# Kernel tuning notes

Measured on AMD Instinct MI355X. Metric: run time of the kernel, lower is better.

The kernel has to match this reference:

```python
import jax, jax.numpy as jnp
import numpy as np

B, LX, LY, D = 8, 2048, 2048, 256

def setup_inputs() -> dict:
    key = jax.random.key(0)
    k1, k2, k3, k4 = jax.random.split(key, 4)
    x = jax.random.normal(k1, (B, LX, D), dtype=jnp.float32)
    y = jax.random.normal(k2, (B, LY, D), dtype=jnp.float32)
    y_mask = jax.random.randint(k3, (B, LY), 0, 2).astype(jnp.bool_)
    W = jax.random.normal(k4, (D, D), dtype=jnp.float32) * (1.0 / np.sqrt(D))
    b = jnp.zeros((D,), dtype=jnp.float32)
    return {"x": x, "y": y, "y_mask": y_mask, "W": W, "b": b}

def reference(x, y, y_mask, W, b):
    # shared linear + relu projection (torch Linear: x @ W.T + b)
    x_proj = jax.nn.relu(jnp.einsum('bld,ed->ble', x, W) + b)  # [B,LX,D]
    y_proj = jax.nn.relu(jnp.einsum('bld,ed->ble', y, W) + b)  # [B,LY,D]
    scores = jnp.einsum('bxd,byd->bxy', x_proj, y_proj)        # [B,LX,LY]
    scores = jnp.where(y_mask[:, None, :], -jnp.inf, scores)
    alpha = jax.nn.softmax(scores, axis=-1)                    # [B,LX,LY]
    return jnp.einsum('bxy,byd->bxd', alpha, y)                # [B,LX,D]
```

## Files before the change

kernel.cpp:

```cpp
#include <hip/hip_runtime.h>

typedef __attribute__((ext_vector_type(8))) short short8;
typedef _Float16 half8 __attribute__((ext_vector_type(8)));
typedef __attribute__((ext_vector_type(4))) float f32x4;
typedef __attribute__((ext_vector_type(4))) unsigned int uint4v;
typedef __attribute__((ext_vector_type(2))) unsigned int uint2v;

#define B_   8
#define LX_  2048
#define LY_  2048
#define D_   256
#define NROW (B_ * LX_)

__device__ __forceinline__ unsigned short f2bf(float f) {
  unsigned u = __builtin_bit_cast(unsigned, f);
  u += 0x7FFF + ((u >> 16) & 1);
  return (unsigned short)(u >> 16);
}
__device__ __forceinline__ float bf2f(unsigned short h) {
  unsigned u = ((unsigned)h) << 16;
  return __builtin_bit_cast(float, u);
}

__global__ __launch_bounds__(256) void prep_kernel(
    const float* __restrict__ W, unsigned short* __restrict__ Whi,
    unsigned short* __restrict__ Wlo,
    const int* __restrict__ MASK, int* __restrict__ CIDX, int* __restrict__ Lc) {
  int t = threadIdx.x;
  if (blockIdx.x >= 8) {
    int base = (blockIdx.x - 8) * 2048 + t * 8;
    f32x4 f0 = *(const f32x4*)(W + base);
    f32x4 f1 = *(const f32x4*)(W + base + 4);
    float v[8] = {f0[0], f0[1], f0[2], f0[3], f1[0], f1[1], f1[2], f1[3]};
    unsigned short h[8], l[8];
    for (int j = 0; j < 8; ++j) {
      h[j] = f2bf(v[j]);
      l[j] = f2bf(v[j] - bf2f(h[j]));
    }
    uint4v vh = {(unsigned)h[0] | ((unsigned)h[1] << 16), (unsigned)h[2] | ((unsigned)h[3] << 16),
                 (unsigned)h[4] | ((unsigned)h[5] << 16), (unsigned)h[6] | ((unsigned)h[7] << 16)};
    uint4v vl = {(unsigned)l[0] | ((unsigned)l[1] << 16), (unsigned)l[2] | ((unsigned)l[3] << 16),
                 (unsigned)l[4] | ((unsigned)l[5] << 16), (unsigned)l[6] | ((unsigned)l[7] << 16)};
    *(uint4v*)(Whi + base) = vh;
    *(uint4v*)(Wlo + base) = vl;
    return;
  }
  __shared__ int s[256];
  int b = blockIdx.x;
  int f[8];
  int cnt = 0;
  for (int k = 0; k < 8; ++k) {
    f[k] = (MASK[b * 2048 + t * 8 + k] == 0) ? 1 : 0;
    cnt += f[k];
  }
  s[t] = cnt;
  __syncthreads();
  for (int off = 1; off < 256; off <<= 1) {
    int v = (t >= off) ? s[t - off] : 0;
    __syncthreads();
    s[t] += v;
    __syncthreads();
  }
  if (t == 255) Lc[b] = s[255];
  int off = s[t] - cnt;
  for (int k = 0; k < 8; ++k) {
    int j = t * 8 + k;
    if (f[k]) CIDX[b * 2048 + (off++)] = j;
  }
}

__global__ __launch_bounds__(256, 2) void projgather_kernel(
    const float* __restrict__ X, const float* __restrict__ Y,
    const float* __restrict__ bias,
    const unsigned short* __restrict__ Whi, const unsigned short* __restrict__ Wlo,
    const int* __restrict__ CIDX, const int* __restrict__ Lc,
    _Float16* __restrict__ XP, _Float16* __restrict__ YPc,
    _Float16* __restrict__ YTc) {
  __shared__ __align__(16) unsigned char smem[51200];
  int t = threadIdx.x;

  if (blockIdx.x >= 512) {
    _Float16 (*tile)[72] = (_Float16(*)[72])smem;
    int id = blockIdx.x - 512;
    int db = id & 3, nb = (id >> 2) & 31, b = id >> 7;
    int lc = Lc[b];
    int end = (lc + 31) & ~31;
    if (nb * 64 >= end) return;
    int nl = t >> 2, ds = t & 3;
    int j = nb * 64 + nl;
    int idx = (j < lc) ? CIDX[b * 2048 + j] : 0;
    const float* src = Y + (size_t)(b * LY_ + idx) * D_ + db * 64 + ds * 16;
    for (int i = 0; i < 4; ++i) {
      f32x4 f = *(const f32x4*)(src + i * 4);
      for (int k = 0; k < 4; ++k) tile[ds * 16 + i * 4 + k][nl] = (_Float16)f[k];
    }
    __syncthreads();
    int dl = t >> 2, nsub = t & 3;
    uint4v v0 = *(const uint4v*)&tile[dl][nsub * 16];
    uint4v v1 = *(const uint4v*)&tile[dl][nsub * 16 + 8];
    _Float16* dst = YTc + (size_t)(b * D_ + db * 64 + dl) * LY_ + nb * 64 + nsub * 16;
    *(uint4v*)(dst) = v0;
    *(uint4v*)(dst + 8) = v1;
    return;
  }

  unsigned short (*Ah)[40] = (unsigned short(*)[40])(smem);
  unsigned short (*Al)[40] = (unsigned short(*)[40])(smem + 5120);
  unsigned short (*Bh)[40] = (unsigned short(*)[40])(smem + 10240);
  unsigned short (*Bl)[40] = (unsigned short(*)[40])(smem + 30720);

  int lane = t & 63, wave = t >> 6;
  int q = lane >> 4, n15 = lane & 15;
  int arow = t >> 2, aseg = t & 3;
  int erow = t >> 2, ec = t & 3;

  bool isX = blockIdx.x < 256;
  int m0 = 0, b = 0, slot0 = 0, lcb = 0;
  const float* arow_ptr;
  if (isX) {
    m0 = blockIdx.x * 64;
    arow_ptr = X + (size_t)(m0 + arow) * D_;
  } else {
    int id = blockIdx.x - 256;
    b = id >> 5;
    int rb = id & 31;
    lcb = Lc[b];
    slot0 = rb * 64;
    if (slot0 >= lcb) return;
    int sl = slot0 + arow;
    int grow = (sl < lcb) ? CIDX[b * 2048 + sl] : 0;
    arow_ptr = Y + (size_t)(b * 2048 + grow) * D_;
  }

  f32x4 acc[4][4];
  for (int mt = 0; mt < 4; ++mt)
    for (int nt = 0; nt < 4; ++nt) acc[mt][nt] = (f32x4){0.f, 0.f, 0.f, 0.f};

  f32x4 pa[2];
  uint4v pbh[4], pbl[4];
#define PROJ_PF(kc)                                                            \
  {                                                                            \
    for (int i = 0; i < 2; ++i)                                                \
      pa[i] = *(const f32x4*)(arow_ptr + (kc) * 32 + (aseg + i * 4) * 4);      \
    for (int p = 0; p < 4; ++p) {                                              \
      int e = p * 64 + erow;                                                   \
      pbh[p] = *(const uint4v*)(Whi + (size_t)e * D_ + (kc) * 32 + ec * 8);    \
      pbl[p] = *(const uint4v*)(Wlo + (size_t)e * D_ + (kc) * 32 + ec * 8);    \
    }                                                                          \
  }

  PROJ_PF(0);

  for (int kc = 0; kc < 8; ++kc) {
    __syncthreads();
    for (int i = 0; i < 2; ++i) {
      int seg = aseg + i * 4;
      f32x4 f = pa[i];
      unsigned short h[4], l[4];
      for (int j = 0; j < 4; ++j) {
        h[j] = f2bf(f[j]);
        l[j] = f2bf(f[j] - bf2f(h[j]));
      }
      uint2v vh = {(unsigned)h[0] | ((unsigned)h[1] << 16),
                   (unsigned)h[2] | ((unsigned)h[3] << 16)};
      uint2v vl = {(unsigned)l[0] | ((unsigned)l[1] << 16),
                   (unsigned)l[2] | ((unsigned)l[3] << 16)};
      *(uint2v*)&Ah[arow][seg * 4] = vh;
      *(uint2v*)&Al[arow][seg * 4] = vl;
    }
    for (int p = 0; p < 4; ++p) {
      int e = p * 64 + erow;
      *(uint4v*)&Bh[e][ec * 8] = pbh[p];
      *(uint4v*)&Bl[e][ec * 8] = pbl[p];
    }
    if (kc < 7) PROJ_PF(kc + 1);
    __syncthreads();

    short8 afh[4], afl[4], bfh[4], bfl[4];
    for (int mt = 0; mt < 4; ++mt) {
      afh[mt] = *(const short8*)&Ah[mt * 16 + n15][q * 8];
      afl[mt] = *(const short8*)&Al[mt * 16 + n15][q * 8];
    }
    for (int nt = 0; nt < 4; ++nt) {
      bfh[nt] = *(const short8*)&Bh[wave * 64 + nt * 16 + n15][q * 8];
      bfl[nt] = *(const short8*)&Bl[wave * 64 + nt * 16 + n15][q * 8];
    }
    for (int mt = 0; mt < 4; ++mt)
      for (int nt = 0; nt < 4; ++nt) {
        acc[mt][nt] = __builtin_amdgcn_mfma_f32_16x16x32_bf16(afh[mt], bfh[nt], acc[mt][nt], 0, 0, 0);
        acc[mt][nt] = __builtin_amdgcn_mfma_f32_16x16x32_bf16(afl[mt], bfh[nt], acc[mt][nt], 0, 0, 0);
        acc[mt][nt] = __builtin_amdgcn_mfma_f32_16x16x32_bf16(afh[mt], bfl[nt], acc[mt][nt], 0, 0, 0);
      }
  }
#undef PROJ_PF

  __syncthreads();
  _Float16 (*epi)[264] = (_Float16(*)[264])smem;
  for (int nt = 0; nt < 4; ++nt) {
    int e = wave * 64 + nt * 16 + n15;
    float bv = bias[e];
    for (int mt = 0; mt < 4; ++mt)
      for (int r = 0; r < 4; ++r) {
        float v = acc[mt][nt][r] + bv;
        v = v > 0.f ? v : 0.f;
        epi[mt * 16 + q * 4 + r][e] = (_Float16)v;
      }
  }
  __syncthreads();
  int row = t >> 2, seg = t & 3;
  bool valid = isX || (slot0 + row < lcb);
  if (valid) {
    _Float16* drp = isX ? (XP + (size_t)(m0 + row) * D_)
                        : (YPc + (size_t)(b * 2048 + slot0 + row) * D_);
    for (int k = 0; k < 8; ++k) {
      uint4v v = *(const uint4v*)&epi[row][seg * 64 + k * 8];
      *(uint4v*)(drp + seg * 64 + k * 8) = v;
    }
  }
}

__global__ __launch_bounds__(256, 2) void flash_kernel(
    const _Float16* __restrict__ XP, const _Float16* __restrict__ YPc,
    const _Float16* __restrict__ YTc, const int* __restrict__ Lc,
    _Float16* __restrict__ PO, float* __restrict__ Pm, float* __restrict__ Pl) {
  __shared__ _Float16 yp_t[32][264];
  __shared__ _Float16 yT_t[256][40];
  __shared__ _Float16 pbuf[4][16][40];

  int t = threadIdx.x;
  int lane = t & 63, wave = t >> 6;
  int q = lane >> 4, n15 = lane & 15;
  int half = blockIdx.x & 1;
  int xb = (blockIdx.x >> 1) & 31;
  int b = blockIdx.x >> 6;
  int row0 = xb * 64 + wave * 16;

  int lc = Lc[b];
  int T  = (lc + 31) >> 5;
  int T0 = (T + 1) >> 1;
  int tstart = half ? T0 : 0;
  int tend   = half ? T  : T0;

  half8 a[8];
  const _Float16* xrow = XP + (size_t)(b * LX_ + row0 + n15) * D_ + q * 8;
  for (int kk = 0; kk < 8; ++kk) a[kk] = *(const half8*)(xrow + kk * 32);

  half8 lones;
  for (int j = 0; j < 8; ++j) lones[j] = (n15 == 0) ? (_Float16)1 : (_Float16)0;

  float m_r[4];
  for (int r = 0; r < 4; ++r) m_r[r] = -1e30f;
  f32x4 lacc = {0.f, 0.f, 0.f, 0.f};
  f32x4 oacc[16];
  for (int dt = 0; dt < 16; ++dt) oacc[dt] = (f32x4){0.f, 0.f, 0.f, 0.f};

  const _Float16* ypb = YPc + (size_t)b * LY_ * D_;
  const _Float16* yTb = YTc + (size_t)b * D_ * LY_;

  uint4v pr[8];
#define PREFETCH(tt)                                                          \
  {                                                                           \
    int y0p = (tt) * 32;                                                      \
    for (int i = 0; i < 4; ++i) {                                             \
      int c = t + i * 256;                                                    \
      pr[i] = *(const uint4v*)(ypb + (size_t)(y0p + (c >> 5)) * D_ + (c & 31) * 8); \
    }                                                                         \
    for (int i = 0; i < 4; ++i) {                                             \
      int c = t + i * 256;                                                    \
      pr[4 + i] = *(const uint4v*)(yTb + (size_t)(c >> 2) * LY_ + y0p + (c & 3) * 8); \
    }                                                                         \
  }

  if (tstart < tend) PREFETCH(tstart);

  for (int tt = tstart; tt < tend; ++tt) {
    int y0 = tt * 32;
    __syncthreads();
    for (int i = 0; i < 4; ++i) {
      int c = t + i * 256;
      *(uint4v*)&yp_t[c >> 5][(c & 31) * 8] = pr[i];
    }
    for (int i = 0; i < 4; ++i) {
      int c = t + i * 256;
      *(uint4v*)&yT_t[c >> 2][(c & 3) * 8] = pr[4 + i];
    }
    if (tt + 1 < tend) PREFETCH(tt + 1);
    __syncthreads();

    f32x4 S0 = {0.f, 0.f, 0.f, 0.f}, S1 = {0.f, 0.f, 0.f, 0.f};
    for (int kk = 0; kk < 8; ++kk) {
      half8 b0 = *(const half8*)&yp_t[n15][kk * 32 + q * 8];
      S0 = __builtin_amdgcn_mfma_f32_16x16x32_f16(a[kk], b0, S0, 0, 0, 0);
    }
    for (int kk = 0; kk < 8; ++kk) {
      half8 b1 = *(const half8*)&yp_t[16 + n15][kk * 32 + q * 8];
      S1 = __builtin_amdgcn_mfma_f32_16x16x32_f16(a[kk], b1, S1, 0, 0, 0);
    }
    bool mk0 = (y0 + n15) >= lc;
    bool mk1 = (y0 + 16 + n15) >= lc;

    float al[4];
    _Float16 ph0[4], ph1[4];
    bool need = false;
    for (int r = 0; r < 4; ++r) {
      float s0 = mk0 ? -1e30f : S0[r];
      float s1 = mk1 ? -1e30f : S1[r];
      float tm = fmaxf(s0, s1);
      tm = fmaxf(tm, __shfl_xor(tm, 1));
      tm = fmaxf(tm, __shfl_xor(tm, 2));
      tm = fmaxf(tm, __shfl_xor(tm, 4));
      tm = fmaxf(tm, __shfl_xor(tm, 8));
      float mn = fmaxf(m_r[r], tm);
      al[r] = __expf(m_r[r] - mn);
      m_r[r] = mn;
      ph0[r] = (_Float16)__expf(s0 - mn);
      ph1[r] = (_Float16)__expf(s1 - mn);
      need = need || (al[r] != 1.0f);
    }
    if (__ballot(need)) {
      for (int dt = 0; dt < 16; ++dt)
        for (int r = 0; r < 4; ++r) oacc[dt][r] *= al[r];
      for (int r = 0; r < 4; ++r) lacc[r] *= al[r];
    }
    for (int r = 0; r < 4; ++r) {
      pbuf[wave][q * 4 + r][n15] = ph0[r];
      pbuf[wave][q * 4 + r][16 + n15] = ph1[r];
    }
    half8 pa = *(const half8*)&pbuf[wave][n15][q * 8];
    lacc = __builtin_amdgcn_mfma_f32_16x16x32_f16(pa, lones, lacc, 0, 0, 0);
    for (int dt = 0; dt < 16; ++dt) {
      half8 bb = *(const half8*)&yT_t[dt * 16 + n15][q * 8];
      oacc[dt] = __builtin_amdgcn_mfma_f32_16x16x32_f16(pa, bb, oacc[dt], 0, 0, 0);
    }
  }
#undef PREFETCH

  size_t prow = (size_t)(half * B_ + b) * LX_ + row0;
  _Float16* po = PO + prow * D_;
  for (int dt = 0; dt < 16; ++dt)
    for (int r = 0; r < 4; ++r)
      po[(size_t)(q * 4 + r) * D_ + dt * 16 + n15] = (_Float16)oacc[dt][r];
  if (n15 == 0) {
    for (int r = 0; r < 4; ++r) {
      Pm[prow + q * 4 + r] = m_r[r];
      Pl[prow + q * 4 + r] = lacc[r];
    }
  }
}

__global__ __launch_bounds__(256) void merge_kernel(
    const _Float16* __restrict__ PO, const float* __restrict__ Pm,
    const float* __restrict__ Pl, float* __restrict__ OUT) {
  int c = blockIdx.x * 256 + threadIdx.x;
  int row = c >> 5, seg = c & 31;
  float m0 = Pm[row], m1 = Pm[NROW + row];
  float l0 = Pl[row], l1 = Pl[NROW + row];
  float m = fmaxf(m0, m1);
  float w0 = __expf(m0 - m), w1 = __expf(m1 - m);
  float inv = 1.0f / (l0 * w0 + l1 * w1);
  const _Float16* p0 = PO + (size_t)row * D_ + seg * 8;
  const _Float16* p1 = p0 + (size_t)NROW * D_;
  half8 a = *(const half8*)p0;
  half8 bsec = *(const half8*)p1;
  float* o = OUT + (size_t)row * D_ + seg * 8;
  f32x4 o0, o1;
  for (int j = 0; j < 4; ++j) o0[j] = ((float)a[j] * w0 + (float)bsec[j] * w1) * inv;
  for (int j = 0; j < 4; ++j) o1[j] = ((float)a[4 + j] * w0 + (float)bsec[4 + j] * w1) * inv;
  *(f32x4*)o = o0;
  *(f32x4*)(o + 4) = o1;
}

extern "C" void kernel_launch(void* const* d_in, const int* in_sizes, int n_in,
                              void* d_out, int out_size, void* d_ws, size_t ws_size,
                              hipStream_t stream) {
  const float* x     = (const float*)d_in[0];
  const float* y     = (const float*)d_in[1];
  const int*   ymask = (const int*)  d_in[2];
  const float* W     = (const float*)d_in[3];
  const float* bias  = (const float*)d_in[4];
  float* out = (float*)d_out;

  char* ws = (char*)d_ws;
  size_t o = 0;
  unsigned short* Whi = (unsigned short*)(ws + o); o += 131072;
  unsigned short* Wlo = (unsigned short*)(ws + o); o += 131072;
  _Float16* XP  = (_Float16*)(ws + o); o += 8388608;
  _Float16* YPc = (_Float16*)(ws + o); o += 8388608;
  _Float16* YTc = (_Float16*)(ws + o); o += 8388608;
  _Float16* PO  = (_Float16*)(ws + o); o += 16777216;
  float* Pm   = (float*)(ws + o); o += 131072;
  float* Pl   = (float*)(ws + o); o += 131072;
  int*   CIDX = (int*)  (ws + o); o += 65536;
  int*   Lc   = (int*)  (ws + o);

  prep_kernel<<<40, 256, 0, stream>>>(W, Whi, Wlo, ymask, CIDX, Lc);
  projgather_kernel<<<1536, 256, 0, stream>>>(x, y, bias, Whi, Wlo, CIDX, Lc,
                                              XP, YPc, YTc);
  flash_kernel<<<512, 256, 0, stream>>>(XP, YPc, YTc, Lc, PO, Pm, Pl);
  merge_kernel<<<2048, 256, 0, stream>>>(PO, Pm, Pl, out);
}
```

Before: 154.8 us.

## Generalize split-KV flash attention to four splits and swizzle transposed-Y LDS tile

Generalizes the key-dimension split in the flash kernel from a fixed 2 to 2^lg partitions. It uses 4 splits, giving 1024 blocks, when the workspace is large enough. The merge kernel now combines an arbitrary number of partial (O, m, l) results. It also drops the padding on the transposed-Y shared tile and applies an XOR swizzle to avoid LDS bank conflicts. More splits should improve occupancy and load balance across CUs, at the cost of more partial-output traffic and merge work.

```diff
diff --git a/kernel.cpp b/kernel.cpp
--- a/kernel.cpp
+++ b/kernel.cpp
@@ -222,24 +222,25 @@
 __global__ __launch_bounds__(256, 2) void flash_kernel(
     const _Float16* __restrict__ XP, const _Float16* __restrict__ YPc,
     const _Float16* __restrict__ YTc, const int* __restrict__ Lc,
-    _Float16* __restrict__ PO, float* __restrict__ Pm, float* __restrict__ Pl) {
-  __shared__ _Float16 yp_t[32][264];
-  __shared__ _Float16 yT_t[256][40];
-  __shared__ _Float16 pbuf[4][16][40];
+    _Float16* __restrict__ PO, float* __restrict__ Pm, float* __restrict__ Pl,
+    int lg) {
+  __shared__ __align__(16) _Float16 yp_t[32][264];
+  __shared__ __align__(16) _Float16 yT_t[256][32];
+  __shared__ __align__(16) _Float16 pbuf[4][16][40];
 
   int t = threadIdx.x;
   int lane = t & 63, wave = t >> 6;
   int q = lane >> 4, n15 = lane & 15;
-  int half = blockIdx.x & 1;
-  int xb = (blockIdx.x >> 1) & 31;
-  int b = blockIdx.x >> 6;
+  int ns = 1 << lg;
+  int half = blockIdx.x & (ns - 1);
+  int xb = (blockIdx.x >> lg) & 31;
+  int b = blockIdx.x >> (lg + 5);
   int row0 = xb * 64 + wave * 16;
 
   int lc = Lc[b];
   int T  = (lc + 31) >> 5;
-  int T0 = (T + 1) >> 1;
-  int tstart = half ? T0 : 0;
-  int tend   = half ? T  : T0;
+  int tstart = (T * half) >> lg;
+  int tend   = (T * (half + 1)) >> lg;
 
   half8 a[8];
   const _Float16* xrow = XP + (size_t)(b * LX_ + row0 + n15) * D_ + q * 8;
@@ -282,7 +283,8 @@
     }
     for (int i = 0; i < 4; ++i) {
       int c = t + i * 256;
-      *(uint4v*)&yT_t[c >> 2][(c & 3) * 8] = pr[4 + i];
+      int rT = c >> 2, pc = (c & 3) ^ (rT & 3);
+      *(uint4v*)&yT_t[rT][pc * 8] = pr[4 + i];
     }
     if (tt + 1 < tend) PREFETCH(tt + 1);
     __syncthreads();
@@ -329,7 +331,8 @@
     half8 pa = *(const half8*)&pbuf[wave][n15][q * 8];
     lacc = __builtin_amdgcn_mfma_f32_16x16x32_f16(pa, lones, lacc, 0, 0, 0);
     for (int dt = 0; dt < 16; ++dt) {
-      half8 bb = *(const half8*)&yT_t[dt * 16 + n15][q * 8];
+      int rT = dt * 16 + n15;
+      half8 bb = *(const half8*)&yT_t[rT][(q ^ (rT & 3)) * 8];
       oacc[dt] = __builtin_amdgcn_mfma_f32_16x16x32_f16(pa, bb, oacc[dt], 0, 0, 0);
     }
   }
@@ -350,22 +353,25 @@
 
 __global__ __launch_bounds__(256) void merge_kernel(
     const _Float16* __restrict__ PO, const float* __restrict__ Pm,
-    const float* __restrict__ Pl, float* __restrict__ OUT) {
+    const float* __restrict__ Pl, float* __restrict__ OUT, int ns) {
   int c = blockIdx.x * 256 + threadIdx.x;
   int row = c >> 5, seg = c & 31;
-  float m0 = Pm[row], m1 = Pm[NROW + row];
-  float l0 = Pl[row], l1 = Pl[NROW + row];
-  float m = fmaxf(m0, m1);
-  float w0 = __expf(m0 - m), w1 = __expf(m1 - m);
-  float inv = 1.0f / (l0 * w0 + l1 * w1);
-  const _Float16* p0 = PO + (size_t)row * D_ + seg * 8;
-  const _Float16* p1 = p0 + (size_t)NROW * D_;
-  half8 a = *(const half8*)p0;
-  half8 bsec = *(const half8*)p1;
+  float m = Pm[row];
+  for (int p = 1; p < ns; ++p) m = fmaxf(m, Pm[p * NROW + row]);
+  float denom = 0.f;
+  f32x4 o0 = {0.f, 0.f, 0.f, 0.f}, o1 = {0.f, 0.f, 0.f, 0.f};
+  for (int p = 0; p < ns; ++p) {
+    float w = __expf(Pm[p * NROW + row] - m);
+    denom += Pl[p * NROW + row] * w;
+    const _Float16* pp = PO + ((size_t)p * NROW + row) * D_ + seg * 8;
+    half8 a = *(const half8*)pp;
+    for (int j = 0; j < 4; ++j) o0[j] += (float)a[j] * w;
+    for (int j = 0; j < 4; ++j) o1[j] += (float)a[4 + j] * w;
+  }
+  float inv = 1.0f / denom;
+  for (int j = 0; j < 4; ++j) o0[j] *= inv;
+  for (int j = 0; j < 4; ++j) o1[j] *= inv;
   float* o = OUT + (size_t)row * D_ + seg * 8;
-  f32x4 o0, o1;
-  for (int j = 0; j < 4; ++j) o0[j] = ((float)a[j] * w0 + (float)bsec[j] * w1) * inv;
-  for (int j = 0; j < 4; ++j) o1[j] = ((float)a[4 + j] * w0 + (float)bsec[4 + j] * w1) * inv;
   *(f32x4*)o = o0;
   *(f32x4*)(o + 4) = o1;
 }
@@ -380,6 +386,14 @@
   const float* bias  = (const float*)d_in[4];
   float* out = (float*)d_out;
 
+  size_t need4 = 262144ull
+               + 3ull * 8388608ull
+               + 4ull * 8388608ull
+               + 2ull * 262144ull
+               + 65536ull + 4096ull;
+  int lg = (ws_size >= need4) ? 2 : 1;
+  int nsplit = 1 << lg;
+
   char* ws = (char*)d_ws;
   size_t o = 0;
   unsigned short* Whi = (unsigned short*)(ws + o); o += 131072;
@@ -387,15 +401,15 @@
   _Float16* XP  = (_Float16*)(ws + o); o += 8388608;
   _Float16* YPc = (_Float16*)(ws + o); o += 8388608;
   _Float16* YTc = (_Float16*)(ws + o); o += 8388608;
-  _Float16* PO  = (_Float16*)(ws + o); o += 16777216;
-  float* Pm   = (float*)(ws + o); o += 131072;
-  float* Pl   = (float*)(ws + o); o += 131072;
+  _Float16* PO  = (_Float16*)(ws + o); o += (size_t)nsplit * 8388608;
+  float* Pm   = (float*)(ws + o); o += (size_t)nsplit * 65536;
+  float* Pl   = (float*)(ws + o); o += (size_t)nsplit * 65536;
   int*   CIDX = (int*)  (ws + o); o += 65536;
   int*   Lc   = (int*)  (ws + o);
 
   prep_kernel<<<40, 256, 0, stream>>>(W, Whi, Wlo, ymask, CIDX, Lc);
   projgather_kernel<<<1536, 256, 0, stream>>>(x, y, bias, Whi, Wlo, CIDX, Lc,
                                               XP, YPc, YTc);
-  flash_kernel<<<512, 256, 0, stream>>>(XP, YPc, YTc, Lc, PO, Pm, Pl);
-  merge_kernel<<<2048, 256, 0, stream>>>(PO, Pm, Pl, out);
-}
+  flash_kernel<<<256 * nsplit, 256, 0, stream>>>(XP, YPc, YTc, Lc, PO, Pm, Pl, lg);
+  merge_kernel<<<2048, 256, 0, stream>>>(PO, Pm, Pl, out, nsplit);
+}
```

Result: slower. 161.7 us (+4.5%).

## Double key tile to 64 rows, swizzle transposed-V LDS, compute row sums in registers

Applied to the files above, without the earlier changes.

The flash kernel now processes 64 key rows per tile instead of 32. This halves the number of barriers and online-softmax rescales per key, and each P fragment now feeds two MFMAs per output tile. The transposed-value tile in LDS uses an XOR swizzle instead of padding to avoid bank conflicts. The row-sum MFMA against a ones vector is replaced by scalar per-lane accumulation plus a final shuffle reduction. The cost is more LDS and prefetch registers per block, which may reduce occupancy, and coarser tail masking.

```diff
diff --git a/kernel.cpp b/kernel.cpp
--- a/kernel.cpp
+++ b/kernel.cpp
@@ -223,9 +223,9 @@
     const _Float16* __restrict__ XP, const _Float16* __restrict__ YPc,
     const _Float16* __restrict__ YTc, const int* __restrict__ Lc,
     _Float16* __restrict__ PO, float* __restrict__ Pm, float* __restrict__ Pl) {
-  __shared__ _Float16 yp_t[32][264];
-  __shared__ _Float16 yT_t[256][40];
-  __shared__ _Float16 pbuf[4][16][40];
+  __shared__ __align__(16) _Float16 yp_t[64][264];
+  __shared__ __align__(16) _Float16 yT_t[256][64];
+  __shared__ __align__(16) _Float16 pbuf[4][16][72];
 
   int t = threadIdx.x;
   int lane = t & 63, wave = t >> 6;
@@ -236,17 +236,13 @@
   int row0 = xb * 64 + wave * 16;
 
   int lc = Lc[b];
-  int T  = (lc + 31) >> 5;
-  int T0 = (T + 1) >> 1;
-  int tstart = half ? T0 : 0;
-  int tend   = half ? T  : T0;
+  int T  = (lc + 63) >> 6;
+  int tstart = (T * half) >> 1;
+  int tend   = (T * (half + 1)) >> 1;
 
   half8 a[8];
   const _Float16* xrow = XP + (size_t)(b * LX_ + row0 + n15) * D_ + q * 8;
   for (int kk = 0; kk < 8; ++kk) a[kk] = *(const half8*)(xrow + kk * 32);
-
-  half8 lones;
-  for (int j = 0; j < 8; ++j) lones[j] = (n15 == 0) ? (_Float16)1 : (_Float16)0;
 
   float m_r[4];
   for (int r = 0; r < 4; ++r) m_r[r] = -1e30f;
@@ -257,80 +253,94 @@
   const _Float16* ypb = YPc + (size_t)b * LY_ * D_;
   const _Float16* yTb = YTc + (size_t)b * D_ * LY_;
 
-  uint4v pr[8];
+  uint4v pr[16];
 #define PREFETCH(tt)                                                          \
   {                                                                           \
-    int y0p = (tt) * 32;                                                      \
-    for (int i = 0; i < 4; ++i) {                                             \
+    int y0p = (tt) * 64;                                                      \
+    for (int i = 0; i < 8; ++i) {                                             \
       int c = t + i * 256;                                                    \
       pr[i] = *(const uint4v*)(ypb + (size_t)(y0p + (c >> 5)) * D_ + (c & 31) * 8); \
     }                                                                         \
-    for (int i = 0; i < 4; ++i) {                                             \
+    for (int i = 0; i < 8; ++i) {                                             \
       int c = t + i * 256;                                                    \
-      pr[4 + i] = *(const uint4v*)(yTb + (size_t)(c >> 2) * LY_ + y0p + (c & 3) * 8); \
+      pr[8 + i] = *(const uint4v*)(yTb + (size_t)(c >> 3) * LY_ + y0p + (c & 7) * 8); \
     }                                                                         \
   }
 
   if (tstart < tend) PREFETCH(tstart);
 
   for (int tt = tstart; tt < tend; ++tt) {
-    int y0 = tt * 32;
-    __syncthreads();
-    for (int i = 0; i < 4; ++i) {
+    int y0 = tt * 64;
+    __syncthreads();
+    for (int i = 0; i < 8; ++i) {
       int c = t + i * 256;
       *(uint4v*)&yp_t[c >> 5][(c & 31) * 8] = pr[i];
     }
-    for (int i = 0; i < 4; ++i) {
+    for (int i = 0; i < 8; ++i) {
       int c = t + i * 256;
-      *(uint4v*)&yT_t[c >> 2][(c & 3) * 8] = pr[4 + i];
+      int rT = c >> 3, pc = (c & 7) ^ (rT & 7);
+      *(uint4v*)&yT_t[rT][pc * 8] = pr[8 + i];
     }
     if (tt + 1 < tend) PREFETCH(tt + 1);
     __syncthreads();
 
     f32x4 S0 = {0.f, 0.f, 0.f, 0.f}, S1 = {0.f, 0.f, 0.f, 0.f};
+    f32x4 S2 = {0.f, 0.f, 0.f, 0.f}, S3 = {0.f, 0.f, 0.f, 0.f};
     for (int kk = 0; kk < 8; ++kk) {
       half8 b0 = *(const half8*)&yp_t[n15][kk * 32 + q * 8];
+      half8 b1 = *(const half8*)&yp_t[16 + n15][kk * 32 + q * 8];
+      half8 b2 = *(const half8*)&yp_t[32 + n15][kk * 32 + q * 8];
+      half8 b3 = *(const half8*)&yp_t[48 + n15][kk * 32 + q * 8];
       S0 = __builtin_amdgcn_mfma_f32_16x16x32_f16(a[kk], b0, S0, 0, 0, 0);
-    }
-    for (int kk = 0; kk < 8; ++kk) {
-      half8 b1 = *(const half8*)&yp_t[16 + n15][kk * 32 + q * 8];
       S1 = __builtin_amdgcn_mfma_f32_16x16x32_f16(a[kk], b1, S1, 0, 0, 0);
+      S2 = __builtin_amdgcn_mfma_f32_16x16x32_f16(a[kk], b2, S2, 0, 0, 0);
+      S3 = __builtin_amdgcn_mfma_f32_16x16x32_f16(a[kk], b3, S3, 0, 0, 0);
     }
     bool mk0 = (y0 + n15) >= lc;
     bool mk1 = (y0 + 16 + n15) >= lc;
-
-    float al[4];
-    _Float16 ph0[4], ph1[4];
+    bool mk2 = (y0 + 32 + n15) >= lc;
+    bool mk3 = (y0 + 48 + n15) >= lc;
+
+    f32x4 alv;
     bool need = false;
+#pragma unroll
     for (int r = 0; r < 4; ++r) {
       float s0 = mk0 ? -1e30f : S0[r];
       float s1 = mk1 ? -1e30f : S1[r];
-      float tm = fmaxf(s0, s1);
+      float s2 = mk2 ? -1e30f : S2[r];
+      float s3 = mk3 ? -1e30f : S3[r];
+      float tm = fmaxf(fmaxf(s0, s1), fmaxf(s2, s3));
       tm = fmaxf(tm, __shfl_xor(tm, 1));
       tm = fmaxf(tm, __shfl_xor(tm, 2));
       tm = fmaxf(tm, __shfl_xor(tm, 4));
       tm = fmaxf(tm, __shfl_xor(tm, 8));
       float mn = fmaxf(m_r[r], tm);
-      al[r] = __expf(m_r[r] - mn);
+      float al = __expf(m_r[r] - mn);
       m_r[r] = mn;
-      ph0[r] = (_Float16)__expf(s0 - mn);
-      ph1[r] = (_Float16)__expf(s1 - mn);
-      need = need || (al[r] != 1.0f);
+      float p0 = __expf(s0 - mn);
+      float p1 = __expf(s1 - mn);
+      float p2 = __expf(s2 - mn);
+      float p3 = __expf(s3 - mn);
+      pbuf[wave][q * 4 + r][n15]      = (_Float16)p0;
+      pbuf[wave][q * 4 + r][16 + n15] = (_Float16)p1;
+      pbuf[wave][q * 4 + r][32 + n15] = (_Float16)p2;
+      pbuf[wave][q * 4 + r][48 + n15] = (_Float16)p3;
+      lacc[r] = lacc[r] * al + (p0 + p1) + (p2 + p3);
+      alv[r] = al;
+      need = need || (al != 1.0f);
     }
     if (__ballot(need)) {
       for (int dt = 0; dt < 16; ++dt)
-        for (int r = 0; r < 4; ++r) oacc[dt][r] *= al[r];
-      for (int r = 0; r < 4; ++r) lacc[r] *= al[r];
-    }
-    for (int r = 0; r < 4; ++r) {
-      pbuf[wave][q * 4 + r][n15] = ph0[r];
-      pbuf[wave][q * 4 + r][16 + n15] = ph1[r];
-    }
-    half8 pa = *(const half8*)&pbuf[wave][n15][q * 8];
-    lacc = __builtin_amdgcn_mfma_f32_16x16x32_f16(pa, lones, lacc, 0, 0, 0);
+        for (int r = 0; r < 4; ++r) oacc[dt][r] *= alv[r];
+    }
+    half8 pa0 = *(const half8*)&pbuf[wave][n15][q * 8];
+    half8 pa1 = *(const half8*)&pbuf[wave][n15][32 + q * 8];
     for (int dt = 0; dt < 16; ++dt) {
-      half8 bb = *(const half8*)&yT_t[dt * 16 + n15][q * 8];
-      oacc[dt] = __builtin_amdgcn_mfma_f32_16x16x32_f16(pa, bb, oacc[dt], 0, 0, 0);
+      int rT = dt * 16 + n15, x = rT & 7;
+      half8 bb0 = *(const half8*)&yT_t[rT][(q ^ x) * 8];
+      half8 bb1 = *(const half8*)&yT_t[rT][((4 + q) ^ x) * 8];
+      oacc[dt] = __builtin_amdgcn_mfma_f32_16x16x32_f16(pa0, bb0, oacc[dt], 0, 0, 0);
+      oacc[dt] = __builtin_amdgcn_mfma_f32_16x16x32_f16(pa1, bb1, oacc[dt], 0, 0, 0);
     }
   }
 #undef PREFETCH
@@ -340,6 +350,14 @@
   for (int dt = 0; dt < 16; ++dt)
     for (int r = 0; r < 4; ++r)
       po[(size_t)(q * 4 + r) * D_ + dt * 16 + n15] = (_Float16)oacc[dt][r];
+  for (int r = 0; r < 4; ++r) {
+    float v = lacc[r];
+    v += __shfl_xor(v, 1);
+    v += __shfl_xor(v, 2);
+    v += __shfl_xor(v, 4);
+    v += __shfl_xor(v, 8);
+    lacc[r] = v;
+  }
   if (n15 == 0) {
     for (int r = 0; r < 4; ++r) {
       Pm[prow + q * 4 + r] = m_r[r];
```

After: 152.6 us. About the same (-1.5%).

## Double-buffer flash tiles, software-pipeline QK, swizzle LDS and workgroup order

Applied to the files above, without the earlier changes.

The flash kernel now double-buffers the Y tiles in shared memory and computes the next tile's QK^T scores while the current tile's softmax and PV run, overlapping MFMA work with exp and shuffle latency. The transposed Y tile loses its row padding and uses an XOR swizzle to avoid LDS bank conflicts. Row sums are accumulated in registers and reduced by shuffles at the end instead of through an extra MFMA per tile, and workgroup indices are remapped for locality. The split between the two halves is also balanced differently. In exchange, the kernel uses more LDS and registers, which may lower occupancy at two blocks per CU.

```diff
diff --git a/kernel.cpp b/kernel.cpp
--- a/kernel.cpp
+++ b/kernel.cpp
@@ -223,30 +223,28 @@
     const _Float16* __restrict__ XP, const _Float16* __restrict__ YPc,
     const _Float16* __restrict__ YTc, const int* __restrict__ Lc,
     _Float16* __restrict__ PO, float* __restrict__ Pm, float* __restrict__ Pl) {
-  __shared__ _Float16 yp_t[32][264];
-  __shared__ _Float16 yT_t[256][40];
-  __shared__ _Float16 pbuf[4][16][40];
+  __shared__ __align__(16) _Float16 yp_t[2][32][264];
+  __shared__ __align__(16) _Float16 yT_t[2][256][32];
+  __shared__ __align__(16) _Float16 pbuf[4][16][40];
 
   int t = threadIdx.x;
   int lane = t & 63, wave = t >> 6;
   int q = lane >> 4, n15 = lane & 15;
-  int half = blockIdx.x & 1;
-  int xb = (blockIdx.x >> 1) & 31;
-  int b = blockIdx.x >> 6;
+  int wg = (int)blockIdx.x;
+  int swz = (wg & 7) * 64 + (wg >> 3);
+  int half = swz & 1;
+  int xb = (swz >> 1) & 31;
+  int b = swz >> 6;
   int row0 = xb * 64 + wave * 16;
 
   int lc = Lc[b];
   int T  = (lc + 31) >> 5;
-  int T0 = (T + 1) >> 1;
-  int tstart = half ? T0 : 0;
-  int tend   = half ? T  : T0;
+  int ts = (T * half) >> 1;
+  int te = (T * (half + 1)) >> 1;
 
   half8 a[8];
   const _Float16* xrow = XP + (size_t)(b * LX_ + row0 + n15) * D_ + q * 8;
   for (int kk = 0; kk < 8; ++kk) a[kk] = *(const half8*)(xrow + kk * 32);
-
-  half8 lones;
-  for (int j = 0; j < 8; ++j) lones[j] = (n15 == 0) ? (_Float16)1 : (_Float16)0;
 
   float m_r[4];
   for (int r = 0; r < 4; ++r) m_r[r] = -1e30f;
@@ -258,7 +256,7 @@
   const _Float16* yTb = YTc + (size_t)b * D_ * LY_;
 
   uint4v pr[8];
-#define PREFETCH(tt)                                                          \
+#define PF(tt)                                                                \
   {                                                                           \
     int y0p = (tt) * 32;                                                      \
     for (int i = 0; i < 4; ++i) {                                             \
@@ -270,76 +268,110 @@
       pr[4 + i] = *(const uint4v*)(yTb + (size_t)(c >> 2) * LY_ + y0p + (c & 3) * 8); \
     }                                                                         \
   }
-
-  if (tstart < tend) PREFETCH(tstart);
-
-  for (int tt = tstart; tt < tend; ++tt) {
+#define STAGE(bi)                                                             \
+  {                                                                           \
+    for (int i = 0; i < 4; ++i) {                                             \
+      int c = t + i * 256;                                                    \
+      *(uint4v*)&yp_t[bi][c >> 5][(c & 31) * 8] = pr[i];                      \
+    }                                                                         \
+    for (int i = 0; i < 4; ++i) {                                             \
+      int c = t + i * 256;                                                    \
+      int rT = c >> 2, pc = (c & 3) ^ (rT & 3);                               \
+      *(uint4v*)&yT_t[bi][rT][pc * 8] = pr[4 + i];                            \
+    }                                                                         \
+  }
+#define QK(bi, S0x, S1x)                                                      \
+  {                                                                           \
+    S0x = (f32x4){0.f, 0.f, 0.f, 0.f};                                        \
+    S1x = (f32x4){0.f, 0.f, 0.f, 0.f};                                        \
+    for (int kk = 0; kk < 8; ++kk) {                                          \
+      half8 b0 = *(const half8*)&yp_t[bi][n15][kk * 32 + q * 8];              \
+      half8 b1 = *(const half8*)&yp_t[bi][16 + n15][kk * 32 + q * 8];         \
+      S0x = __builtin_amdgcn_mfma_f32_16x16x32_f16(a[kk], b0, S0x, 0, 0, 0);  \
+      S1x = __builtin_amdgcn_mfma_f32_16x16x32_f16(a[kk], b1, S1x, 0, 0, 0);  \
+    }                                                                         \
+  }
+
+  f32x4 S0c = {0.f, 0.f, 0.f, 0.f}, S1c = {0.f, 0.f, 0.f, 0.f};
+  f32x4 S0n = {0.f, 0.f, 0.f, 0.f}, S1n = {0.f, 0.f, 0.f, 0.f};
+
+  if (ts < te) {
+    PF(ts);
+    STAGE(ts & 1);
+    if (ts + 1 < te) PF(ts + 1);
+    __syncthreads();
+    QK(ts & 1, S0c, S1c);
+    if (ts + 1 < te) STAGE((ts + 1) & 1);
+    if (ts + 2 < te) PF(ts + 2);
+    __syncthreads();
+  }
+
+  for (int tt = ts; tt < te; ++tt) {
     int y0 = tt * 32;
-    __syncthreads();
-    for (int i = 0; i < 4; ++i) {
-      int c = t + i * 256;
-      *(uint4v*)&yp_t[c >> 5][(c & 31) * 8] = pr[i];
-    }
-    for (int i = 0; i < 4; ++i) {
-      int c = t + i * 256;
-      *(uint4v*)&yT_t[c >> 2][(c & 3) * 8] = pr[4 + i];
-    }
-    if (tt + 1 < tend) PREFETCH(tt + 1);
-    __syncthreads();
-
-    f32x4 S0 = {0.f, 0.f, 0.f, 0.f}, S1 = {0.f, 0.f, 0.f, 0.f};
-    for (int kk = 0; kk < 8; ++kk) {
-      half8 b0 = *(const half8*)&yp_t[n15][kk * 32 + q * 8];
-      S0 = __builtin_amdgcn_mfma_f32_16x16x32_f16(a[kk], b0, S0, 0, 0, 0);
-    }
-    for (int kk = 0; kk < 8; ++kk) {
-      half8 b1 = *(const half8*)&yp_t[16 + n15][kk * 32 + q * 8];
-      S1 = __builtin_amdgcn_mfma_f32_16x16x32_f16(a[kk], b1, S1, 0, 0, 0);
-    }
+    int cur = tt & 1, nxt = cur ^ 1;
+
+    if (tt + 1 < te) QK(nxt, S0n, S1n);
     bool mk0 = (y0 + n15) >= lc;
     bool mk1 = (y0 + 16 + n15) >= lc;
-
-    float al[4];
-    _Float16 ph0[4], ph1[4];
+    f32x4 alv;
     bool need = false;
+#pragma unroll
     for (int r = 0; r < 4; ++r) {
-      float s0 = mk0 ? -1e30f : S0[r];
-      float s1 = mk1 ? -1e30f : S1[r];
+      float s0 = mk0 ? -1e30f : S0c[r];
+      float s1 = mk1 ? -1e30f : S1c[r];
       float tm = fmaxf(s0, s1);
       tm = fmaxf(tm, __shfl_xor(tm, 1));
       tm = fmaxf(tm, __shfl_xor(tm, 2));
       tm = fmaxf(tm, __shfl_xor(tm, 4));
       tm = fmaxf(tm, __shfl_xor(tm, 8));
       float mn = fmaxf(m_r[r], tm);
-      al[r] = __expf(m_r[r] - mn);
+      float al = __expf(m_r[r] - mn);
       m_r[r] = mn;
-      ph0[r] = (_Float16)__expf(s0 - mn);
-      ph1[r] = (_Float16)__expf(s1 - mn);
-      need = need || (al[r] != 1.0f);
+      float p0 = __expf(s0 - mn);
+      float p1 = __expf(s1 - mn);
+      pbuf[wave][q * 4 + r][n15]      = (_Float16)p0;
+      pbuf[wave][q * 4 + r][16 + n15] = (_Float16)p1;
+      lacc[r] = lacc[r] * al + p0 + p1;
+      alv[r] = al;
+      need = need || (al != 1.0f);
     }
     if (__ballot(need)) {
       for (int dt = 0; dt < 16; ++dt)
-        for (int r = 0; r < 4; ++r) oacc[dt][r] *= al[r];
-      for (int r = 0; r < 4; ++r) lacc[r] *= al[r];
-    }
-    for (int r = 0; r < 4; ++r) {
-      pbuf[wave][q * 4 + r][n15] = ph0[r];
-      pbuf[wave][q * 4 + r][16 + n15] = ph1[r];
+        for (int r = 0; r < 4; ++r) oacc[dt][r] *= alv[r];
     }
     half8 pa = *(const half8*)&pbuf[wave][n15][q * 8];
-    lacc = __builtin_amdgcn_mfma_f32_16x16x32_f16(pa, lones, lacc, 0, 0, 0);
     for (int dt = 0; dt < 16; ++dt) {
-      half8 bb = *(const half8*)&yT_t[dt * 16 + n15][q * 8];
+      int rT = dt * 16 + n15;
+      half8 bb = *(const half8*)&yT_t[cur][rT][((q ^ (rT & 3))) * 8];
       oacc[dt] = __builtin_amdgcn_mfma_f32_16x16x32_f16(pa, bb, oacc[dt], 0, 0, 0);
     }
-  }
-#undef PREFETCH
+
+    __syncthreads();
+    if (tt + 2 < te) {
+      STAGE(cur);
+      if (tt + 3 < te) PF(tt + 3);
+    }
+    __syncthreads();
+    S0c = S0n;
+    S1c = S1n;
+  }
+#undef PF
+#undef STAGE
+#undef QK
 
   size_t prow = (size_t)(half * B_ + b) * LX_ + row0;
   _Float16* po = PO + prow * D_;
   for (int dt = 0; dt < 16; ++dt)
     for (int r = 0; r < 4; ++r)
       po[(size_t)(q * 4 + r) * D_ + dt * 16 + n15] = (_Float16)oacc[dt][r];
+  for (int r = 0; r < 4; ++r) {
+    float v = lacc[r];
+    v += __shfl_xor(v, 1);
+    v += __shfl_xor(v, 2);
+    v += __shfl_xor(v, 4);
+    v += __shfl_xor(v, 8);
+    lacc[r] = v;
+  }
   if (n15 == 0) {
     for (int r = 0; r < 4; ++r) {
       Pm[prow + q * 4 + r] = m_r[r];
```

Result: no change. 155.4 us (+0.4%).
